# Performance work log

Hardware: AMD Instinct MI355X
Metric: run time of the kernel (lower is better)

Reference implementation:

```python
import jax, jax.numpy as jnp
import numpy as np

C = 256      # embed_dim
GROUP = 2    # conv groups
K = 3        # kernel/pool size
K2 = K * K
OG = 8       # offset groups (hard-coded in Similarity_cal)
NEX = 3      # exemplars per image (out_conv expects group*3*4 channels)


def conv2d(x, w, b, pad):
    y = jax.lax.conv_general_dilated(x, w, (1, 1), [(pad, pad), (pad, pad)],
                                     dimension_numbers=("NCHW", "OIHW", "NCHW"))
    return y + b[None, :, None, None]


def ln_c(x, g, b, eps=1e-5):
    # LayerNorm over the channel axis of NCHW (torch permutes to NHWC, LN, permute back)
    mu = x.mean(axis=1, keepdims=True)
    var = ((x - mu) ** 2).mean(axis=1, keepdims=True)
    return (x - mu) / jnp.sqrt(var + eps) * g[None, :, None, None] + b[None, :, None, None]


def bilinear_gather(img, py, px):
    # img [Cg,H,W]; py,px [K2,H,W] -> samples [Cg,K2,H,W], zero outside borders
    Cg, H, W = img.shape
    y0f = jnp.floor(py); x0f = jnp.floor(px)
    wy = py - y0f; wx = px - x0f
    y0 = y0f.astype(jnp.int32); x0 = x0f.astype(jnp.int32)
    flat = img.reshape(Cg, H * W)

    def corner(yy, xx, w):
        valid = (yy >= 0) & (yy < H) & (xx >= 0) & (xx < W)
        idx = jnp.clip(yy, 0, H - 1) * W + jnp.clip(xx, 0, W - 1)
        v = jnp.take(flat, idx.reshape(-1), axis=1).reshape(Cg, K2, H, W)
        return v * (w * valid)[None]

    return (corner(y0, x0, (1 - wy) * (1 - wx)) + corner(y0, x0 + 1, (1 - wy) * wx)
            + corner(y0 + 1, x0, wy * (1 - wx)) + corner(y0 + 1, x0 + 1, wy * wx))


def deform_conv(x, offset, mask, weight, dilation):
    # x [C,H,W]; offset [2*OG*K2,H,W]; mask [OG*K2,H,W] (softmaxed); weight [NEX*GROUP, C//GROUP, K, K]
    Cc, H, W = x.shape
    pad = (K - 1) * dilation // 2
    off = offset.reshape(OG, K2, 2, H, W)  # (dy, dx) per offset-group / tap
    kk = jnp.arange(K, dtype=x.dtype)
    ky = jnp.repeat(kk, K) * dilation - pad  # [K2]
    kx = jnp.tile(kk, K) * dilation - pad
    ii = jnp.arange(H, dtype=x.dtype)
    jj = jnp.arange(W, dtype=x.dtype)
    py = ii[None, None, :, None] + ky[None, :, None, None] + off[:, :, 0]  # [OG,K2,H,W]
    px = jj[None, None, None, :] + kx[None, :, None, None] + off[:, :, 1]
    xg = x.reshape(OG, Cc // OG, H, W)
    samp = jax.vmap(bilinear_gather)(xg, py, px)              # [OG,Cg,K2,H,W]
    samp = samp * mask.reshape(OG, 1, K2, H, W)               # modulation
    samp = samp.reshape(GROUP, Cc // GROUP, K2, H, W)
    wR = weight.reshape(NEX * GROUP, Cc // GROUP, K2)
    gidx = jnp.arange(NEX * GROUP) // NEX                     # out-channel -> conv group
    return jnp.einsum("rck,rckhw->rhw", wR, samp[gidx])       # [NEX*GROUP,H,W]


def forward(querys_feat, supports_feat, in_w, in_b, ln_g, ln_b, out_w, out_b,
            offw1, offb1, mskw1, mskb1, offw2, offb2, mskw2, mskb2,
            offw4, offb4, mskw4, mskb4):
    B = querys_feat.shape[0]
    q = ln_c(conv2d(querys_feat, in_w, in_b, 0), ln_g, ln_b)                 # [B,C,H,W]
    s = supports_feat.reshape(B * NEX, C, K, K)
    s = ln_c(conv2d(s, in_w, in_b, 0), ln_g, ln_b).reshape(B, NEX, C, K, K)

    def offs(wo, bo, wm, bm):
        o = conv2d(q, wo, bo, (K - 1) // 2)
        m = jax.nn.softmax(conv2d(q, wm, bm, (K - 1) // 2), axis=1)  # softmax over all OG*K2 channels
        return o, m

    o1, m1 = offs(offw1, offb1, mskw1, mskb1)
    o2, m2 = offs(offw2, offb2, mskw2, mskb2)
    o4, m4 = offs(offw4, offb4, mskw4, mskb4)

    def per_sample(qi, si, o1i, m1i, o2i, m2i, o4i, m4i):
        w = si.reshape(NEX * GROUP, C // GROUP, K, K)         # dynamic per-exemplar kernels
        pooled = si.max(axis=(2, 3)).reshape(NEX * GROUP, C // GROUP)
        gidx = jnp.arange(NEX * GROUP) // NEX
        qg = qi.reshape(GROUP, C // GROUP, *qi.shape[1:])
        sim0 = jnp.einsum("rc,rchw->rhw", pooled, qg[gidx])   # grouped 1x1 conv branch
        d1 = deform_conv(qi, o1i, m1i, w, 1)
        d2 = deform_conv(qi, o2i, m2i, w, 2)
        d4 = deform_conv(qi, o4i, m4i, w, 4)
        return jnp.concatenate([sim0, d1, d2, d4], axis=0)    # [GROUP*3*4, H, W]

    sim = jax.vmap(per_sample)(q, s, o1, m1, o2, m2, o4, m4)
    return conv2d(sim, out_w, out_b, 0)                        # [B,C,H,W]


def setup_inputs() -> dict:
    key = jax.random.key(0)
    ks = jax.random.split(key, 20)
    B, H, W = 2, 96, 96
    inp = {
        "querys_feat": jax.random.normal(ks[0], (B, C, H, W), jnp.float32),
        "supports_feat": jax.random.normal(ks[1], (B, NEX, C, K, K), jnp.float32),
        "in_w": jax.random.normal(ks[2], (C, C, 1, 1), jnp.float32) / 16.0,
        "in_b": jax.random.normal(ks[3], (C,), jnp.float32) * 0.02,
        "ln_g": jnp.ones((C,), jnp.float32),
        "ln_b": jnp.zeros((C,), jnp.float32),
        "out_w": jax.random.normal(ks[4], (C, GROUP * 3 * 4, 1, 1), jnp.float32) * 0.2,
        "out_b": jax.random.normal(ks[5], (C,), jnp.float32) * 0.02,
    }
    i = 6
    for d in (1, 2, 4):
        inp[f"offw{d}"] = jax.random.normal(ks[i], (2 * OG * K2, C, K, K), jnp.float32) * 0.01; i += 1
        inp[f"offb{d}"] = jax.random.normal(ks[i], (2 * OG * K2,), jnp.float32) * 0.1; i += 1
        inp[f"mskw{d}"] = jax.random.normal(ks[i], (OG * K2, C, K, K), jnp.float32) * 0.02; i += 1
        inp[f"mskb{d}"] = jax.random.normal(ks[i], (OG * K2,), jnp.float32) * 0.1; i += 1
    return inp


def reference(querys_feat, supports_feat, in_w, in_b, ln_g, ln_b, out_w, out_b,
              offw1, offb1, mskw1, mskb1, offw2, offb2, mskw2, mskb2,
              offw4, offb4, mskw4, mskb4):
    return forward(querys_feat, supports_feat, in_w, in_b, ln_g, ln_b, out_w, out_b,
                   offw1, offb1, mskw1, mskb1, offw2, offb2, mskw2, mskb2,
                   offw4, offb4, mskw4, mskb4)
```

## Files before the change

kernel.cpp:

```cpp
#include <hip/hip_runtime.h>
#include <hip/hip_bf16.h>
#include <math.h>

#define HH 96
#define WWID 96
#define HW 9216
#define CC 256
#define BB 2
#define PROW 104
#define PCOL 128
#define PPX (PROW * PCOL)

typedef float f32x4 __attribute__((ext_vector_type(4)));
typedef _Float16 f16x8 __attribute__((ext_vector_type(8)));
typedef _Float16 h2v __attribute__((ext_vector_type(2)));

__device__ inline unsigned int pack2h(float a, float b) {
  unsigned short ua = __builtin_bit_cast(unsigned short, (_Float16)a);
  unsigned short ub = __builtin_bit_cast(unsigned short, (_Float16)b);
  return (unsigned int)ua | ((unsigned int)ub << 16);
}

#if defined(__has_builtin)
#if __has_builtin(__builtin_amdgcn_fdot2)
#define FDOT2(a, b, c) __builtin_amdgcn_fdot2((a), (b), (c), false)
#endif
#endif
#ifndef FDOT2
#define FDOT2(a, b, c) ((c) + (float)(a).x * (float)(b).x + (float)(a).y * (float)(b).y)
#endif

__device__ inline void gload_lds16(const void* g, void* l) {
  __builtin_amdgcn_global_load_lds(
      (const __attribute__((address_space(1))) void*)g,
      (__attribute__((address_space(3))) void*)l, 16, 0, 0);
}

__global__ void k_prep(const float* __restrict__ in_w, float* __restrict__ wT,
                       const float* __restrict__ ow1, const float* __restrict__ ob1,
                       const float* __restrict__ mw1, const float* __restrict__ mb1,
                       const float* __restrict__ ow2, const float* __restrict__ ob2,
                       const float* __restrict__ mw2, const float* __restrict__ mb2,
                       const float* __restrict__ ow4, const float* __restrict__ ob4,
                       const float* __restrict__ mw4, const float* __restrict__ mb4,
                       _Float16* __restrict__ Whf, float* __restrict__ Ball) {
  int bx = blockIdx.x;
  int t = threadIdx.x;
  if (bx < 256) {
    wT[bx * CC + t] = in_w[t * CC + bx];
    return;
  }
  int idx = (bx - 256) * 256 + t;
  if (idx >= 3 * 256 * 2304) return;
  int d = idx / (256 * 2304);
  int rem = idx - d * 256 * 2304;
  int co = rem / 2304;
  int k = rem - co * 2304;
  int j = k >> 8, ci = k & 255;
  const float* ow = d == 0 ? ow1 : (d == 1 ? ow2 : ow4);
  const float* mw = d == 0 ? mw1 : (d == 1 ? mw2 : mw4);
  float v = 0.f;
  if (co < 144) v = ow[co * 2304 + ci * 9 + j];
  else if (co < 216) v = mw[(co - 144) * 2304 + ci * 9 + j];
  Whf[idx] = (_Float16)v;
  if (idx < 768) {
    int dd = idx >> 8, cc = idx & 255;
    const float* obv = dd == 0 ? ob1 : (dd == 1 ? ob2 : ob4);
    const float* mbv = dd == 0 ? mb1 : (dd == 1 ? mb2 : mb4);
    float bv = 0.f;
    if (cc < 144) bv = obv[cc];
    else if (cc < 216) bv = mbv[cc - 144];
    Ball[idx] = bv;
  }
}

__global__ void k_conv1_ln_q(const float* __restrict__ qin, const float* __restrict__ wT,
                             const float* __restrict__ in_b, const float* __restrict__ ln_g,
                             const float* __restrict__ ln_b, const float* __restrict__ pooled,
                             _Float16* __restrict__ qpad, float* __restrict__ sim) {
  int bx = blockIdx.x;
  int b = bx / 288;
  int hw0 = (bx % 288) * 32;
  int t = threadIdx.x;
  int lane = t & 63;
  int wv_id = t >> 6;
  __shared__ float xs[32 * 260];
  const float* qb = qin + (size_t)b * CC * HW;
  #pragma unroll
  for (int i = 0; i < 32; ++i) {
    int idx = t + i * 256;
    int p = idx & 31;
    int k = idx >> 5;
    xs[p * 260 + k] = qb[k * HW + hw0 + p];
  }
  __syncthreads();
  float acc[8][4];
  #pragma unroll
  for (int p = 0; p < 8; ++p) { acc[p][0]=0.f; acc[p][1]=0.f; acc[p][2]=0.f; acc[p][3]=0.f; }
  const float4* wT4 = (const float4*)wT;
  int p0 = wv_id * 8;
  for (int k = 0; k < 256; k += 4) {
    float4 w0 = wT4[(k + 0) * 64 + lane];
    float4 w1 = wT4[(k + 1) * 64 + lane];
    float4 w2 = wT4[(k + 2) * 64 + lane];
    float4 w3 = wT4[(k + 3) * 64 + lane];
    #pragma unroll
    for (int p = 0; p < 8; ++p) {
      float4 xv = *(const float4*)&xs[(p0 + p) * 260 + k];
      acc[p][0] += w0.x * xv.x + w1.x * xv.y + w2.x * xv.z + w3.x * xv.w;
      acc[p][1] += w0.y * xv.x + w1.y * xv.y + w2.y * xv.z + w3.y * xv.w;
      acc[p][2] += w0.z * xv.x + w1.z * xv.y + w2.z * xv.z + w3.z * xv.w;
      acc[p][3] += w0.w * xv.x + w1.w * xv.y + w2.w * xv.z + w3.w * xv.w;
    }
  }
  float4 bb = ((const float4*)in_b)[lane];
  float4 g4 = ((const float4*)ln_g)[lane];
  float4 b4 = ((const float4*)ln_b)[lane];
  int lg = lane >> 5;
  int lc = lane & 31;
  const float4* pp = (const float4*)(pooled + (size_t)b * 768 + (lg * 3) * 128);
  float4 pr0 = pp[lc];
  float4 pr1 = pp[32 + lc];
  float4 pr2 = pp[64 + lc];
  #pragma unroll
  for (int p = 0; p < 8; ++p) {
    float y0 = acc[p][0] + bb.x, y1 = acc[p][1] + bb.y;
    float y2 = acc[p][2] + bb.z, y3 = acc[p][3] + bb.w;
    float s1 = y0 + y1 + y2 + y3;
    float s2 = y0*y0 + y1*y1 + y2*y2 + y3*y3;
    #pragma unroll
    for (int off = 32; off; off >>= 1) { s1 += __shfl_xor(s1, off); s2 += __shfl_xor(s2, off); }
    float mu = s1 * (1.f / 256.f);
    float rstd = rsqrtf(s2 * (1.f / 256.f) - mu * mu + 1e-5f);
    float4 o;
    o.x = (y0 - mu) * rstd * g4.x + b4.x;
    o.y = (y1 - mu) * rstd * g4.y + b4.y;
    o.z = (y2 - mu) * rstd * g4.z + b4.z;
    o.w = (y3 - mu) * rstd * g4.w + b4.w;
    int hw = hw0 + p0 + p;
    int hh = hw / 96, ww = hw - hh * 96;
    int ppx = (hh + 4) * PCOL + ww + 4;
    struct alignas(8) h4 { _Float16 h[4]; };
    h4 oh;
    oh.h[0] = (_Float16)o.x; oh.h[1] = (_Float16)o.y;
    oh.h[2] = (_Float16)o.z; oh.h[3] = (_Float16)o.w;
    *(h4*)(qpad + ((size_t)b * PPX + ppx) * CC + lane * 4) = oh;
    float r0 = pr0.x * o.x + pr0.y * o.y + pr0.z * o.z + pr0.w * o.w;
    float r1 = pr1.x * o.x + pr1.y * o.y + pr1.z * o.z + pr1.w * o.w;
    float r2 = pr2.x * o.x + pr2.y * o.y + pr2.z * o.z + pr2.w * o.w;
    #pragma unroll
    for (int off = 16; off; off >>= 1) {
      r0 += __shfl_xor(r0, off);
      r1 += __shfl_xor(r1, off);
      r2 += __shfl_xor(r2, off);
    }
    if (lc == 0) {
      size_t base = ((size_t)b * 24 + lg * 3) * HW + hw;
      sim[base] = r0;
      sim[base + HW] = r1;
      sim[base + 2 * HW] = r2;
    }
  }
}

__global__ void k_conv1_ln_s(const float* __restrict__ sup, const float* __restrict__ wT,
                             const float* __restrict__ in_b, const float* __restrict__ ln_g,
                             const float* __restrict__ ln_b, float* __restrict__ s_ln,
                             float* __restrict__ pooled) {
  int img = blockIdx.x;
  int t = threadIdx.x;
  __shared__ float xs[2304];
  __shared__ float red1[256], red2[256];
  #pragma unroll
  for (int p = 0; p < 9; ++p) xs[t * 9 + p] = sup[(size_t)img * 2304 + t * 9 + p];
  __syncthreads();
  float acc[9];
  #pragma unroll
  for (int p = 0; p < 9; ++p) acc[p] = 0.f;
  for (int k = 0; k < 256; ++k) {
    float wv = wT[k * CC + t];
    #pragma unroll
    for (int p = 0; p < 9; ++p) acc[p] += wv * xs[k * 9 + p];
  }
  float bias = in_b[t];
  #pragma unroll
  for (int p = 0; p < 9; ++p) acc[p] += bias;
  float g = ln_g[t], be = ln_b[t];
  float vals[9];
  #pragma unroll
  for (int p = 0; p < 9; ++p) {
    red1[t] = acc[p]; red2[t] = acc[p] * acc[p];
    __syncthreads();
    for (int s = 128; s > 0; s >>= 1) {
      if (t < s) { red1[t] += red1[t + s]; red2[t] += red2[t + s]; }
      __syncthreads();
    }
    float mu = red1[0] * (1.f / 256.f);
    float var = red2[0] * (1.f / 256.f) - mu * mu;
    float rstd = rsqrtf(var + 1e-5f);
    vals[p] = (acc[p] - mu) * rstd * g + be;
    __syncthreads();
  }
  #pragma unroll
  for (int p = 0; p < 9; ++p) s_ln[(size_t)img * 2304 + t * 9 + p] = vals[p];
  float mx = vals[0];
  #pragma unroll
  for (int p = 1; p < 9; ++p) mx = fmaxf(mx, vals[p]);
  int b = img / 3, e = img % 3;
  pooled[((size_t)b * 6 + e * 2 + (t >> 7)) * 128 + (t & 127)] = mx;
}


#define BAR() __builtin_amdgcn_s_barrier()
#define SCHEDB() __builtin_amdgcn_sched_barrier(0)
#define VMCNT(N) asm volatile("s_waitcnt vmcnt(" #N ")" ::: "memory")

#define MMA_ONE(M, N, S, QM, QN) \
  acc[(QM)*4+(M)][(QN)*2+(N)] = __builtin_amdgcn_mfma_f32_16x16x32_f16( \
      af[M][S], bf[(QN)*2+(N)][S], acc[(QM)*4+(M)][(QN)*2+(N)], 0, 0, 0);

#define MMA_Q(QM, QN) { \
  __builtin_amdgcn_s_setprio(1); \
  MMA_ONE(0,0,0,QM,QN) MMA_ONE(1,0,0,QM,QN) MMA_ONE(2,0,0,QM,QN) MMA_ONE(3,0,0,QM,QN) \
  MMA_ONE(0,1,0,QM,QN) MMA_ONE(1,1,0,QM,QN) MMA_ONE(2,1,0,QM,QN) MMA_ONE(3,1,0,QM,QN) \
  MMA_ONE(0,0,1,QM,QN) MMA_ONE(1,0,1,QM,QN) MMA_ONE(2,0,1,QM,QN) MMA_ONE(3,0,1,QM,QN) \
  MMA_ONE(0,1,1,QM,QN) MMA_ONE(1,1,1,QM,QN) MMA_ONE(2,1,1,QM,QN) MMA_ONE(3,1,1,QM,QN) \
  __builtin_amdgcn_s_setprio(0); }

#define LDA(BUF, QM) { \
  const char* p_ = smemB + (BUF) * 65536 + (wm * 128 + (QM) * 64 + l15) * 128; \
  af[0][0] = *(const f16x8*)(p_ + 0*2048 + rc0); af[0][1] = *(const f16x8*)(p_ + 0*2048 + rc1); \
  af[1][0] = *(const f16x8*)(p_ + 1*2048 + rc0); af[1][1] = *(const f16x8*)(p_ + 1*2048 + rc1); \
  af[2][0] = *(const f16x8*)(p_ + 2*2048 + rc0); af[2][1] = *(const f16x8*)(p_ + 2*2048 + rc1); \
  af[3][0] = *(const f16x8*)(p_ + 3*2048 + rc0); af[3][1] = *(const f16x8*)(p_ + 3*2048 + rc1); }

#define LDB(BUF, QN) { \
  const char* p_ = smemB + (BUF) * 65536 + 32768 + (wn * 64 + (QN) * 32 + l15) * 128; \
  bf[(QN)*2+0][0] = *(const f16x8*)(p_ + 0*2048 + rc0); bf[(QN)*2+0][1] = *(const f16x8*)(p_ + 0*2048 + rc1); \
  bf[(QN)*2+1][0] = *(const f16x8*)(p_ + 1*2048 + rc0); bf[(QN)*2+1][1] = *(const f16x8*)(p_ + 1*2048 + rc1); }

#define STAGEA(TILE, Q) { \
  gload_lds16(aBase + (size_t)((Q) * 64) * 2304 + (TILE) * 64, \
              smemB + ((TILE) & 1) * 65536 + (((Q) * 64 + wv * 8) * 128)); \
  gload_lds16(aBase + (size_t)(128 + (Q) * 64) * 2304 + (TILE) * 64, \
              smemB + ((TILE) & 1) * 65536 + ((128 + (Q) * 64 + wv * 8) * 128)); }

#define STAGEB(TILE, Q, PPX0, PPX1) { \
  int j_ = (TILE) >> 2; \
  int offp_ = (j_ / 3 - 1) * PCOL + (j_ % 3) - 1; \
  int cb_ = ((TILE) & 3) * 64; \
  int rs_ = (wv >> 2) * 64 + (Q) * 32 + (wv & 3) * 8; \
  gload_lds16(bBase + (size_t)((PPX0) + offp_) * CC + cb_, \
              smemB + ((TILE) & 1) * 65536 + 32768 + (rs_ * 128)); \
  gload_lds16(bBase + (size_t)((PPX1) + offp_) * CC + cb_, \
              smemB + ((TILE) & 1) * 65536 + 32768 + ((128 + rs_) * 128)); }

__global__ void __launch_bounds__(512) k_conv3_mfma8(
    const _Float16* __restrict__ qpad, const _Float16* __restrict__ Whf,
    const float* __restrict__ Ball, unsigned int* __restrict__ taprec) {
  int nb = blockIdx.x;
  int z = blockIdx.y;
  int d = z >> 1, b = z & 1;
  int t = threadIdx.x;
  int lane = t & 63, wv = t >> 6;
  int wm = wv >> 2, wn = wv & 3;
  int quad = lane >> 4, l15 = lane & 15;
  int l8 = lane >> 3, c7 = lane & 7;

  __shared__ _Float16 __attribute__((aligned(16))) smem[65536];
  char* smemB = (char*)smem;

  const _Float16* Wd = Whf + (size_t)d * 256 * 2304;
  const _Float16* qb = qpad + (size_t)b * PPX * CC;

  int scol = ((c7 ^ l8) << 3);
  int rc0 = ((quad ^ (l15 & 7)) << 4);
  int rc1 = (((4 | quad) ^ (l15 & 7)) << 4);

  const _Float16* aBase = Wd + (size_t)(wv * 8 + l8) * 2304 + scol;
  const _Float16* bBase = qb + scol;

  int ppx00, ppx01, ppx10, ppx11;
  {
    int rbase = (wv >> 2) * 64 + (wv & 3) * 8 + l8;
    int px, hh, ww;
    px = nb * 256 + rbase;             hh = px / 96; ww = px - hh * 96; ppx00 = (hh + 4) * PCOL + ww + 4;
    px = nb * 256 + 128 + rbase;       hh = px / 96; ww = px - hh * 96; ppx01 = (hh + 4) * PCOL + ww + 4;
    px = nb * 256 + 32 + rbase;        hh = px / 96; ww = px - hh * 96; ppx10 = (hh + 4) * PCOL + ww + 4;
    px = nb * 256 + 160 + rbase;       hh = px / 96; ww = px - hh * 96; ppx11 = (hh + 4) * PCOL + ww + 4;
  }

  f32x4 acc[8][4];
  #pragma unroll
  for (int i = 0; i < 8; ++i)
    #pragma unroll
    for (int j = 0; j < 4; ++j) acc[i][j] = (f32x4){0.f, 0.f, 0.f, 0.f};

  f16x8 af[4][2], bf[4][2];

  STAGEA(0, 0);
  STAGEB(0, 1, ppx10, ppx11);
  STAGEA(0, 1);
  STAGEB(0, 0, ppx00, ppx01);
  STAGEA(1, 0);
  STAGEB(1, 1, ppx10, ppx11);
  VMCNT(4);
  BAR();
  SCHEDB();

  #pragma unroll 1
  for (int ii = 0; ii < 17; ++ii) {
    int ta = 2 * ii + 1, tb = 2 * ii + 2, tc = 2 * ii + 3;
    LDA(0, 0) LDB(0, 0)
    STAGEA(ta, 1);
    BAR(); MMA_Q(0, 0); BAR();
    LDB(0, 1)
    STAGEB(ta, 0, ppx00, ppx01);
    BAR(); MMA_Q(0, 1); BAR();
    LDA(0, 1)
    STAGEA(tb, 0);
    BAR(); MMA_Q(1, 1); BAR();
    STAGEB(tb, 1, ppx10, ppx11);
    VMCNT(4);
    BAR(); SCHEDB(); MMA_Q(1, 0); BAR();
    LDA(1, 0) LDB(1, 0)
    STAGEA(tb, 1);
    BAR(); MMA_Q(0, 0); BAR();
    LDB(1, 1)
    STAGEB(tb, 0, ppx00, ppx01);
    BAR(); MMA_Q(0, 1); BAR();
    LDA(1, 1)
    STAGEA(tc, 0);
    BAR(); MMA_Q(1, 1); BAR();
    STAGEB(tc, 1, ppx10, ppx11);
    VMCNT(4);
    BAR(); SCHEDB(); MMA_Q(1, 0); BAR();
  }

  LDA(0, 0) LDB(0, 0)
  STAGEA(35, 1);
  BAR(); MMA_Q(0, 0); BAR();
  LDB(0, 1)
  STAGEB(35, 0, ppx00, ppx01);
  BAR(); MMA_Q(0, 1); BAR();
  LDA(0, 1)
  BAR(); MMA_Q(1, 1); BAR();
  VMCNT(0);
  BAR(); SCHEDB(); MMA_Q(1, 0); BAR();
  LDA(1, 0) LDB(1, 0)
  BAR(); MMA_Q(0, 0); BAR();
  LDB(1, 1)
  BAR(); MMA_Q(0, 1); BAR();
  LDA(1, 1)
  BAR(); MMA_Q(1, 1); BAR();
  MMA_Q(1, 0);

  BAR();
  float* cs = (float*)smemB;
  const float* Bd = Ball + d * 256;
  unsigned int* tzo = taprec + (size_t)z * 72 * HW * 3;
  int sub = t & 7;
  int pxq = t >> 3;
  int dil = 1 << d;

  #pragma unroll 1
  for (int H = 0; H < 2; ++H) {
    if ((wn >> 1) == H) {
      #pragma unroll
      for (int mi = 0; mi < 8; ++mi) {
        int c2 = wm * 128 + mi * 16 + quad * 4;
        if (c2 < 216) {
          float4 bq = *(const float4*)(Bd + c2);
          #pragma unroll
          for (int ni = 0; ni < 4; ++ni) {
            int pl = (wn & 1) * 64 + ni * 16 + l15;
            f32x4 v = acc[mi][ni];
            float* cp = &cs[pl * 225 + c2];
            cp[0] = v[0] + bq.x; cp[1] = v[1] + bq.y;
            cp[2] = v[2] + bq.z; cp[3] = v[3] + bq.w;
          }
        }
      }
    }
    BAR();
    #pragma unroll 1
    for (int p = 0; p < 2; ++p) {
      int pl = p * 64 + pxq;
      int px = nb * 256 + H * 128 + pl;
      const float* cr = &cs[pl * 225];
      float lg[9];
      float mx = -1e30f;
      #pragma unroll
      for (int j = 0; j < 9; ++j) {
        lg[j] = cr[144 + sub + 8 * j];
        mx = fmaxf(mx, lg[j]);
      }
      mx = fmaxf(mx, __shfl_xor(mx, 1));
      mx = fmaxf(mx, __shfl_xor(mx, 2));
      mx = fmaxf(mx, __shfl_xor(mx, 4));
      float s = 0.f;
      #pragma unroll
      for (int j = 0; j < 9; ++j) s += __expf(lg[j] - mx);
      s += __shfl_xor(s, 1);
      s += __shfl_xor(s, 2);
      s += __shfl_xor(s, 4);
      float rinv = 1.f / s;
      int h = px / WWID, w = px - h * WWID;
      int k = sub;
      #pragma unroll
      for (int j = 0; j < 9; ++j) {
        int tk = sub + 8 * j;
        float dy = cr[tk * 2 + 0];
        float dx = cr[tk * 2 + 1];
        float m = __expf(lg[j] - mx) * rinv;
        float py = (float)(h + (k / 3) * dil - dil) + dy;
        float pxx = (float)(w + (k % 3) * dil - dil) + dx;
        float y0f = floorf(py), x0f = floorf(pxx);
        int y0 = (int)y0f, x0 = (int)x0f;
        float wy = py - y0f, wx = pxx - x0f;
        bool vy0 = (unsigned)y0 < 96u, vy1 = (unsigned)(y0 + 1) < 96u;
        bool vx0 = (unsigned)x0 < 96u, vx1 = (unsigned)(x0 + 1) < 96u;
        float w00 = (vy0 && vx0) ? (1.f - wy) * (1.f - wx) * m : 0.f;
        float w01 = (vy0 && vx1) ? (1.f - wy) * wx * m : 0.f;
        float w10 = (vy1 && vx0) ? wy * (1.f - wx) * m : 0.f;
        float w11 = (vy1 && vx1) ? wy * wx * m : 0.f;
        int iy = min(max(y0 + 4, 0), 102);
        int ix = min(max(x0 + 4, 0), 126);
        unsigned int* r = tzo + ((size_t)tk * HW + px) * 3;
        r[0] = pack2h(w00, w01);
        r[1] = pack2h(w10, w11);
        r[2] = (unsigned int)(iy * PCOL + ix);
        k += 8; if (k >= 9) k -= 9;
      }
    }
    BAR();
  }
}

#define DO_P(U0, U1, IDX, P) { \
  h2v u0_ = __builtin_bit_cast(h2v, (U0)); \
  h2v u1_ = __builtin_bit_cast(h2v, (U1)); \
  const h2v* b0_ = qc + (size_t)(IDX) * 128; \
  h2v q00_ = b0_[0], q01_ = b0_[128]; \
  h2v q10_ = b0_[16384], q11_ = b0_[16384 + 128]; \
  h2v s_ = q00_ * (h2v){u0_.x, u0_.x} + q01_ * (h2v){u0_.y, u0_.y} \
         + q10_ * (h2v){u1_.x, u1_.x} + q11_ * (h2v){u1_.y, u1_.y}; \
  acc[P][0] = FDOT2(wr0, s_, acc[P][0]); \
  acc[P][1] = FDOT2(wr1, s_, acc[P][1]); \
  acc[P][2] = FDOT2(wr2, s_, acc[P][2]); }

__global__ void __launch_bounds__(256) k_deform(
    const _Float16* __restrict__ qpad, const unsigned int* __restrict__ taprec,
    const float* __restrict__ s_ln, float* __restrict__ sim) {
  int bid = blockIdx.x;
  int slab = bid & 7;
  int j = bid >> 3;
  int z = j / 72;
  int rem = j - z * 72;
  int yhalf = rem / 36;
  int segin = rem - yhalf * 36;
  int seg = slab * 36 + segin;
  int d_idx = z >> 1, b = z & 1;
  int t = threadIdx.x;
  int g = t >> 5, lane = t & 31;
  int half16 = lane >> 4, l16 = lane & 15;
  __shared__ _Float16 wh[9 * 384];
  __shared__ unsigned int rlds[36 * 96];
  int px0 = seg * 32;
  int tkbase = yhalf * 36;
  const unsigned int* tz = taprec + (size_t)z * 72 * HW * 3;
  for (int i2 = t; i2 < 3456; i2 += 256) {
    int c = i2 / 9, k = i2 % 9;
    wh[k * 384 + c] = (_Float16)s_ln[(size_t)b * 6912 + yhalf * 3456 + i2];
  }
  for (int i2 = t; i2 < 3456; i2 += 256) {
    int tko = i2 / 96, dw = i2 - tko * 96;
    rlds[i2] = tz[((size_t)(tkbase + tko) * HW + px0) * 3 + dw];
  }
  __syncthreads();
  int pg = g * 4;
  int pxb = px0 + pg;
  const unsigned int* whd = (const unsigned int*)wh;
  const _Float16* qb = qpad + (size_t)b * PPX * CC;

  float acc[4][3];
  #pragma unroll
  for (int p = 0; p < 4; ++p)
    #pragma unroll
    for (int r = 0; r < 3; ++r) acc[p][r] = 0.f;

  #pragma unroll 1
  for (int ogp = 0; ogp < 2; ++ogp) {
    int og = yhalf * 4 + ogp * 2 + half16;
    int qch = og * 32 + l16 * 2;
    int wcol = qch - yhalf * 128;
    int tko = (ogp * 2 + half16) * 9;
    const h2v* qc = (const h2v*)(qb + qch);
    #pragma unroll 3
    for (int k = 0; k < 9; ++k) {
      const unsigned int* rr = &rlds[(tko + k) * 96 + pg * 3];
      h2v wr0 = __builtin_bit_cast(h2v, whd[(k * 384 + 0 + wcol) >> 1]);
      h2v wr1 = __builtin_bit_cast(h2v, whd[(k * 384 + 128 + wcol) >> 1]);
      h2v wr2 = __builtin_bit_cast(h2v, whd[(k * 384 + 256 + wcol) >> 1]);
      DO_P(rr[0], rr[1], rr[2], 0)
      DO_P(rr[3], rr[4], rr[5], 1)
      DO_P(rr[6], rr[7], rr[8], 2)
      DO_P(rr[9], rr[10], rr[11], 3)
    }
  }

  #pragma unroll
  for (int p = 0; p < 4; ++p) {
    #pragma unroll
    for (int r = 0; r < 3; ++r) {
      float v = acc[p][r];
      #pragma unroll
      for (int off = 16; off; off >>= 1) v += __shfl_down(v, off, 32);
      if (lane == 0)
        sim[((size_t)b * 24 + 6 + 6 * d_idx + yhalf * 3 + r) * HW + pxb + p] = v;
    }
  }
}

__global__ void k_outconv(const float* __restrict__ sim, const float* __restrict__ out_w,
                          const float* __restrict__ out_b, float* __restrict__ out) {
  int hw = blockIdx.x * 256 + threadIdx.x;
  int co = blockIdx.y, b = blockIdx.z;
  const float* simb = sim + (size_t)b * 24 * HW;
  float a = out_b[co];
  #pragma unroll
  for (int r = 0; r < 24; ++r) a += out_w[co * 24 + r] * simb[(size_t)r * HW + hw];
  out[((size_t)b * CC + co) * HW + hw] = a;
}

extern "C" void kernel_launch(void* const* d_in, const int* in_sizes, int n_in,
                              void* d_out, int out_size, void* d_ws, size_t ws_size,
                              hipStream_t stream) {
  const float* querys = (const float*)d_in[0];
  const float* sup    = (const float*)d_in[1];
  const float* in_w   = (const float*)d_in[2];
  const float* in_b   = (const float*)d_in[3];
  const float* ln_g   = (const float*)d_in[4];
  const float* ln_b   = (const float*)d_in[5];
  const float* out_w  = (const float*)d_in[6];
  const float* out_b  = (const float*)d_in[7];
  const float* ow1 = (const float*)d_in[8];
  const float* ob1 = (const float*)d_in[9];
  const float* mw1 = (const float*)d_in[10];
  const float* mb1 = (const float*)d_in[11];
  const float* ow2 = (const float*)d_in[12];
  const float* ob2 = (const float*)d_in[13];
  const float* mw2 = (const float*)d_in[14];
  const float* mb2 = (const float*)d_in[15];
  const float* ow4 = (const float*)d_in[16];
  const float* ob4 = (const float*)d_in[17];
  const float* mw4 = (const float*)d_in[18];
  const float* mb4 = (const float*)d_in[19];
  float* out = (float*)d_out;

  float* ws_f   = (float*)d_ws;
  float* wT     = ws_f;
  _Float16* Whf = (_Float16*)(wT + 65536);
  float* Ball   = (float*)(Whf + 3 * 256 * 2304);
  _Float16* qpad = (_Float16*)(Ball + 1024);
  float* s_ln   = (float*)(qpad + (size_t)BB * PPX * CC);
  float* pooled = s_ln + 13824;
  unsigned int* taprec = (unsigned int*)(pooled + 1536);
  float* sim    = (float*)(taprec + (size_t)6 * 72 * HW * 3);

  hipMemsetAsync(qpad, 0, (size_t)BB * PPX * CC * sizeof(_Float16), stream);
  k_prep<<<dim3(256 + 6912), dim3(256), 0, stream>>>(
      in_w, wT, ow1, ob1, mw1, mb1, ow2, ob2, mw2, mb2, ow4, ob4, mw4, mb4, Whf, Ball);
  k_conv1_ln_s<<<dim3(6), dim3(256), 0, stream>>>(sup, wT, in_b, ln_g, ln_b, s_ln, pooled);
  k_conv1_ln_q<<<dim3(576), dim3(256), 0, stream>>>(querys, wT, in_b, ln_g, ln_b, pooled, qpad, sim);
  k_conv3_mfma8<<<dim3(36, 6), dim3(512), 0, stream>>>(qpad, Whf, Ball, taprec);
  k_deform<<<dim3(3456), dim3(256), 0, stream>>>(qpad, taprec, s_ln, sim);
  k_outconv<<<dim3(36, 256, BB), dim3(256), 0, stream>>>(sim, out_w, out_b, out);
}
```

Before: 350.9 us.

## Use wave-shuffle LN reduction, vectorized LDS tap loads, and 4-channel outconv blocking

Three unrelated micro-optimizations. The support LayerNorm switches from a 9x tree reduction in shared memory with many barriers to warp shuffles plus one barrier. The deform kernel reads tap records as three 128-bit LDS loads instead of twelve scalar loads. The output 1x1 conv computes four output channels per thread, so each sim value is reused four times and the grid shrinks by four.

```diff
diff --git a/kernel.cpp b/kernel.cpp
--- a/kernel.cpp
+++ b/kernel.cpp
@@ -169,8 +169,10 @@
                              float* __restrict__ pooled) {
   int img = blockIdx.x;
   int t = threadIdx.x;
+  int wv = t >> 6;
+  int lane = t & 63;
   __shared__ float xs[2304];
-  __shared__ float red1[256], red2[256];
+  __shared__ float r1s[4][9], r2s[4][9];
   #pragma unroll
   for (int p = 0; p < 9; ++p) xs[t * 9 + p] = sup[(size_t)img * 2304 + t * 9 + p];
   __syncthreads();
@@ -178,28 +180,32 @@
   #pragma unroll
   for (int p = 0; p < 9; ++p) acc[p] = 0.f;
   for (int k = 0; k < 256; ++k) {
-    float wv = wT[k * CC + t];
-    #pragma unroll
-    for (int p = 0; p < 9; ++p) acc[p] += wv * xs[k * 9 + p];
+    float wv_ = wT[k * CC + t];
+    #pragma unroll
+    for (int p = 0; p < 9; ++p) acc[p] += wv_ * xs[k * 9 + p];
   }
   float bias = in_b[t];
   #pragma unroll
   for (int p = 0; p < 9; ++p) acc[p] += bias;
+  #pragma unroll
+  for (int p = 0; p < 9; ++p) {
+    float s1 = acc[p];
+    float s2 = acc[p] * acc[p];
+    #pragma unroll
+    for (int off = 32; off; off >>= 1) { s1 += __shfl_xor(s1, off); s2 += __shfl_xor(s2, off); }
+    if (lane == 0) { r1s[wv][p] = s1; r2s[wv][p] = s2; }
+  }
+  __syncthreads();
   float g = ln_g[t], be = ln_b[t];
   float vals[9];
   #pragma unroll
   for (int p = 0; p < 9; ++p) {
-    red1[t] = acc[p]; red2[t] = acc[p] * acc[p];
-    __syncthreads();
-    for (int s = 128; s > 0; s >>= 1) {
-      if (t < s) { red1[t] += red1[t + s]; red2[t] += red2[t + s]; }
-      __syncthreads();
-    }
-    float mu = red1[0] * (1.f / 256.f);
-    float var = red2[0] * (1.f / 256.f) - mu * mu;
+    float s1 = r1s[0][p] + r1s[1][p] + r1s[2][p] + r1s[3][p];
+    float s2 = r2s[0][p] + r2s[1][p] + r2s[2][p] + r2s[3][p];
+    float mu = s1 * (1.f / 256.f);
+    float var = s2 * (1.f / 256.f) - mu * mu;
     float rstd = rsqrtf(var + 1e-5f);
     vals[p] = (acc[p] - mu) * rstd * g + be;
-    __syncthreads();
   }
   #pragma unroll
   for (int p = 0; p < 9; ++p) s_ln[(size_t)img * 2304 + t * 9 + p] = vals[p];
@@ -465,7 +471,7 @@
   int g = t >> 5, lane = t & 31;
   int half16 = lane >> 4, l16 = lane & 15;
   __shared__ _Float16 wh[9 * 384];
-  __shared__ unsigned int rlds[36 * 96];
+  __shared__ unsigned int __attribute__((aligned(16))) rlds[36 * 96];
   int px0 = seg * 32;
   int tkbase = yhalf * 36;
   const unsigned int* tz = taprec + (size_t)z * 72 * HW * 3;
@@ -498,14 +504,17 @@
     const h2v* qc = (const h2v*)(qb + qch);
     #pragma unroll 3
     for (int k = 0; k < 9; ++k) {
-      const unsigned int* rr = &rlds[(tko + k) * 96 + pg * 3];
+      const uint4* rr4 = (const uint4*)&rlds[(tko + k) * 96 + pg * 3];
+      uint4 ra = rr4[0];
+      uint4 rb = rr4[1];
+      uint4 rc = rr4[2];
       h2v wr0 = __builtin_bit_cast(h2v, whd[(k * 384 + 0 + wcol) >> 1]);
       h2v wr1 = __builtin_bit_cast(h2v, whd[(k * 384 + 128 + wcol) >> 1]);
       h2v wr2 = __builtin_bit_cast(h2v, whd[(k * 384 + 256 + wcol) >> 1]);
-      DO_P(rr[0], rr[1], rr[2], 0)
-      DO_P(rr[3], rr[4], rr[5], 1)
-      DO_P(rr[6], rr[7], rr[8], 2)
-      DO_P(rr[9], rr[10], rr[11], 3)
+      DO_P(ra.x, ra.y, ra.z, 0)
+      DO_P(ra.w, rb.x, rb.y, 1)
+      DO_P(rb.z, rb.w, rc.x, 2)
+      DO_P(rc.y, rc.z, rc.w, 3)
     }
   }
 
@@ -525,12 +534,26 @@
 __global__ void k_outconv(const float* __restrict__ sim, const float* __restrict__ out_w,
                           const float* __restrict__ out_b, float* __restrict__ out) {
   int hw = blockIdx.x * 256 + threadIdx.x;
-  int co = blockIdx.y, b = blockIdx.z;
+  int coq = blockIdx.y * 4;
+  int b = blockIdx.z;
   const float* simb = sim + (size_t)b * 24 * HW;
-  float a = out_b[co];
-  #pragma unroll
-  for (int r = 0; r < 24; ++r) a += out_w[co * 24 + r] * simb[(size_t)r * HW + hw];
-  out[((size_t)b * CC + co) * HW + hw] = a;
+  float a0 = out_b[coq + 0];
+  float a1 = out_b[coq + 1];
+  float a2 = out_b[coq + 2];
+  float a3 = out_b[coq + 3];
+  #pragma unroll
+  for (int r = 0; r < 24; ++r) {
+    float sv = simb[(size_t)r * HW + hw];
+    a0 += out_w[(coq + 0) * 24 + r] * sv;
+    a1 += out_w[(coq + 1) * 24 + r] * sv;
+    a2 += out_w[(coq + 2) * 24 + r] * sv;
+    a3 += out_w[(coq + 3) * 24 + r] * sv;
+  }
+  size_t base = ((size_t)b * CC + coq) * HW + hw;
+  out[base] = a0;
+  out[base + HW] = a1;
+  out[base + 2 * HW] = a2;
+  out[base + 3 * HW] = a3;
 }
 
 extern "C" void kernel_launch(void* const* d_in, const int* in_sizes, int n_in,
@@ -575,5 +598,5 @@
   k_conv1_ln_q<<<dim3(576), dim3(256), 0, stream>>>(querys, wT, in_b, ln_g, ln_b, pooled, qpad, sim);
   k_conv3_mfma8<<<dim3(36, 6), dim3(512), 0, stream>>>(qpad, Whf, Ball, taprec);
   k_deform<<<dim3(3456), dim3(256), 0, stream>>>(qpad, taprec, s_ln, sim);
-  k_outconv<<<dim3(36, 256, BB), dim3(256), 0, stream>>>(sim, out_w, out_b, out);
-}
+  k_outconv<<<dim3(36, 64, BB), dim3(256), 0, stream>>>(sim, out_w, out_b, out);
+}
```

Result: faster. 341.9 us (-2.6%).
